# Kernel optimization log

Measured on AMD Instinct MI355X. Metric: run time of the kernel, lower is better.

The kernel has to match this reference:

```python
import jax, jax.numpy as jnp
import numpy as np

B, T, C, H = 4, 4096, 512, 64

def setup_inputs() -> dict:
    key = jax.random.key(0)
    kx, kk, kq, kv = jax.random.split(key, 4)
    return {
        "x": jax.random.normal(kx, (B, T, C), dtype=jnp.float32),
        "Wk": jax.random.normal(kk, (C, H), dtype=jnp.float32) * (C ** -0.5),
        "Wq": jax.random.normal(kq, (C, H), dtype=jnp.float32) * (C ** -0.5),
        "Wv": jax.random.normal(kv, (C, H), dtype=jnp.float32) * (C ** -0.5),
    }

def reference(x, Wk, Wq, Wv):
    # x: [B, T, C]; bias-free projections to head_size H
    k = x @ Wk  # [B, T, H]
    q = x @ Wq  # [B, T, H]
    v = x @ Wv  # [B, T, H]
    channels = x.shape[-1]
    # NOTE: original scales by channels**-0.5 (embedding dim), not head_size
    scale = jnp.asarray(channels, x.dtype) ** -0.5
    wei = jnp.einsum("bth,bsh->bts", q, k) * scale  # [B, T, T]
    t = x.shape[1]
    causal = jnp.tril(jnp.ones((t, t), dtype=bool))
    wei = jnp.where(causal, wei, -jnp.inf)
    wei = jax.nn.softmax(wei, axis=-1)
    out = jnp.einsum("bts,bsh->bth", wei, v)  # [B, T, H]
    return out
```

## Files before the change

kernel.cpp:

```cpp
#include <hip/hip_runtime.h>


typedef __attribute__((ext_vector_type(8))) __bf16 bf16x8;
typedef __attribute__((ext_vector_type(8))) unsigned short u16x8;
typedef __attribute__((ext_vector_type(4))) float f32x4;

#define B_ 4
#define T_ 4096
#define C_ 512
#define H_ 64
#define BT (B_ * T_)

#define QSCALE (0.04419417382415922f * 1.4426950408889634f)

__device__ __forceinline__ unsigned short f2bf(float f) {
    unsigned int u = __builtin_bit_cast(unsigned int, f);
    u += 0x7fffu + ((u >> 16) & 1u);
    return (unsigned short)(u >> 16);
}

__device__ __forceinline__ unsigned int pkbf(float hi, float lo) {
    return __builtin_amdgcn_perm(__builtin_bit_cast(unsigned int, hi),
                                 __builtin_bit_cast(unsigned int, lo), 0x07060302u);
}

__device__ __forceinline__ float bf2f_lo(unsigned int u) {
    return __builtin_bit_cast(float, u << 16);
}
__device__ __forceinline__ float bf2f_hi(unsigned int u) {
    return __builtin_bit_cast(float, u & 0xffff0000u);
}

__device__ __forceinline__ f32x4 mfma16(bf16x8 a, bf16x8 b, f32x4 c) {
    return __builtin_amdgcn_mfma_f32_16x16x32_bf16(a, b, c, 0, 0, 0);
}

__device__ __forceinline__ void gload_lds16(const void* g, void* lds_uniform) {
    __builtin_amdgcn_global_load_lds(
        (const __attribute__((address_space(1))) unsigned int*)g,
        (__attribute__((address_space(3))) unsigned int*)lds_uniform, 16, 0, 0);
}

__global__ __launch_bounds__(256) void wt_kernel(const float* __restrict__ Wk,
                                                 const float* __restrict__ Wq,
                                                 const float* __restrict__ Wv,
                                                 unsigned short* __restrict__ Wtp) {
    int gid = blockIdx.x * 256 + threadIdx.x;
    int fidx = gid >> 9;
    int li = gid & 511;
    int lane = li >> 3, j = li & 7;
    int m3 = fidx / 64;
    int rem = fidx & 63;
    int nt = rem >> 4, kc = rem & 15;
    int h = nt * 16 + (lane & 15);
    int c = kc * 32 + (lane >> 4) * 8 + j;
    const float* W = (m3 == 0) ? Wk : ((m3 == 1) ? Wq : Wv);
    Wtp[gid] = f2bf(W[c * H_ + h]);
}

__global__ __launch_bounds__(256, 3) void proj_kernel(const float* __restrict__ x,
                                                      const unsigned short* __restrict__ Wtp,
                                                      unsigned short* __restrict__ Kf,
                                                      unsigned short* __restrict__ Qf,
                                                      unsigned short* __restrict__ Vf) {
    __shared__ __align__(16) char smem[2 * 64 * 52 * 4];
    float* Mg = (float*)smem;
    unsigned short* Ks_l = (unsigned short*)smem;
    unsigned short* Qs_l = Ks_l + 32 * 68;
    unsigned short* Vt_l = Qs_l + 32 * 68;

    const int tid = threadIdx.x;
    const int t0 = blockIdx.x * 32;
    const int wave = tid >> 6;
    const int ws = wave & 1;
    const int wh = wave >> 1;
    const int lane = tid & 63;
    const int lane15 = lane & 15;
    const int quad = lane >> 4;

    f32x4 acc[12];
#pragma unroll
    for (int i = 0; i < 12; ++i) acc[i] = (f32x4){0.f, 0.f, 0.f, 0.f};

    const float* xrow = x + (long)(t0 + ws * 16 + lane15) * C_;
    const unsigned short* wbase = Wtp + lane * 8;

    bf16x8 wf[12];
    float4 xa0[2], xa1[2];
    {
        const int kc0 = wh * 8;
        xa0[0] = *(const float4*)(xrow + kc0 * 32 + quad * 8);
        xa1[0] = *(const float4*)(xrow + kc0 * 32 + quad * 8 + 4);
        xa0[1] = *(const float4*)(xrow + (kc0 + 1) * 32 + quad * 8);
        xa1[1] = *(const float4*)(xrow + (kc0 + 1) * 32 + quad * 8 + 4);
#pragma unroll
        for (int i = 0; i < 12; ++i)
            wf[i] = *(const bf16x8*)(wbase + ((i * 16 + kc0) << 9));
    }

#pragma unroll
    for (int kk = 0; kk < 8; ++kk) {
        const int kc = wh * 8 + kk;
        const int cur = kk & 1;
        u16x8 t;
        t[0] = f2bf(xa0[cur].x); t[1] = f2bf(xa0[cur].y);
        t[2] = f2bf(xa0[cur].z); t[3] = f2bf(xa0[cur].w);
        t[4] = f2bf(xa1[cur].x); t[5] = f2bf(xa1[cur].y);
        t[6] = f2bf(xa1[cur].z); t[7] = f2bf(xa1[cur].w);
        bf16x8 a = __builtin_bit_cast(bf16x8, t);
        if (kk < 6) {
            xa0[cur] = *(const float4*)(xrow + (kc + 2) * 32 + quad * 8);
            xa1[cur] = *(const float4*)(xrow + (kc + 2) * 32 + quad * 8 + 4);
        }
        __builtin_amdgcn_s_setprio(1);
#pragma unroll
        for (int i = 0; i < 12; ++i) {
            acc[i] = mfma16(a, wf[i], acc[i]);
            if (kk < 7)
                wf[i] = *(const bf16x8*)(wbase + ((i * 16 + kc + 1) << 9));
        }
        __builtin_amdgcn_s_setprio(0);
    }

    if (wh == 1) {
        float* mg = Mg + (ws * 64 + lane) * 52;
#pragma unroll
        for (int i = 0; i < 12; ++i) *(f32x4*)(mg + i * 4) = acc[i];
    }
    __syncthreads();
    if (wh == 0) {
        const float* mg = Mg + (ws * 64 + lane) * 52;
#pragma unroll
        for (int i = 0; i < 12; ++i) acc[i] += *(const f32x4*)(mg + i * 4);
    }
    __syncthreads();

    if (wh == 0) {
#pragma unroll
        for (int nt = 0; nt < 4; ++nt) {
            int col = nt * 16 + lane15;
#pragma unroll
            for (int r = 0; r < 4; ++r) {
                int row_l = ws * 16 + quad * 4 + r;
                Ks_l[row_l * 68 + col] = f2bf(acc[0 * 4 + nt][r]);
                Qs_l[row_l * 68 + col] = f2bf(acc[1 * 4 + nt][r] * QSCALE);
                Vt_l[col * 34 + row_l] = f2bf(acc[2 * 4 + nt][r]);
            }
        }
    }
    __syncthreads();

    const int b = t0 >> 12;
    const int tloc = t0 & 4095;
    const int st = wave >> 1, kk = wave & 1;
    const long gs = (long)(b * 256 + (tloc >> 4) + st);
    bf16x8 kv = *(const bf16x8*)&Ks_l[(st * 16 + lane15) * 68 + kk * 32 + quad * 8];
    *(bf16x8*)&Kf[(gs * 2 + kk) * 512 + lane * 8] = kv;
    bf16x8 qv = *(const bf16x8*)&Qs_l[(st * 16 + lane15) * 68 + kk * 32 + quad * 8];
    *(bf16x8*)&Qf[(gs * 2 + kk) * 512 + lane * 8] = qv;
    const int hf = wave;
    const int vkk = (tloc >> 5) & 1;
    bf16x8 vv = *(const bf16x8*)&Vt_l[(hf * 16 + lane15) * 34 + quad * 8];
    const long sb = (long)(b * 64 + (tloc >> 6));
    *(bf16x8*)&Vf[(sb * 8 + hf * 2 + vkk) * 512 + lane * 8] = vv;
}

#define PSP 72

__global__ __launch_bounds__(256, 3) void attn_kernel(const unsigned short* __restrict__ Qf,
                                                      const unsigned short* __restrict__ Kf,
                                                      const unsigned short* __restrict__ Vf,
                                                      unsigned short* __restrict__ Opb,
                                                      float* __restrict__ lp,
                                                      float* __restrict__ out) {
    __shared__ __align__(16) unsigned short KV[2][8192];
    __shared__ __align__(16) unsigned short Ps[8][16 * PSP];

    const int tid = threadIdx.x;
    const int wave = tid >> 6;
    const int lane = tid & 63;
    const int lane15 = lane & 15;
    const int quad = lane >> 4;
    const int b = blockIdx.y;

    const int z = 143 - blockIdx.x;
    int g = (int)((__builtin_sqrtf(2.0f * (float)z + 1.0f) - 1.0f) * 0.5f);
    while (2 * (g + 1) * (g + 2) <= z) ++g;
    while (2 * g * (g + 1) > z) --g;
    const int idx = z - 2 * g * (g + 1);
    const int qmt = g * 4 + idx / (g + 1);
    const int chunk = idx % (g + 1);
    const int ntt = min(8, 2 * qmt + 2 - chunk * 8);
    const int t0k = chunk * 8;
    const int dt0 = 2 * qmt, dt1 = 2 * qmt + 1;
    const int qg0 = qmt * 128 + wave * 16 + lane15;

    const long gq = (long)(b * 256 + qmt * 8 + wave);
    const unsigned short* qb = Qf + gq * 1024 + lane * 8;
    const bf16x8 qf00 = *(const bf16x8*)qb;
    const bf16x8 qf01 = *(const bf16x8*)(qb + 512);
    const bf16x8 qf10 = *(const bf16x8*)(qb + 4096);
    const bf16x8 qf11 = *(const bf16x8*)(qb + 4096 + 512);

    f32x4 o0[4], o1[4];
    f32x4 lv0 = (f32x4){0.f, 0.f, 0.f, 0.f};
    f32x4 lv1 = (f32x4){0.f, 0.f, 0.f, 0.f};
#pragma unroll
    for (int hf = 0; hf < 4; ++hf) {
        o0[hf] = (f32x4){0.f, 0.f, 0.f, 0.f};
        o1[hf] = (f32x4){0.f, 0.f, 0.f, 0.f};
    }

    const char* kbase = (const char*)Kf + ((long)(b * 256) << 11);
    const char* vbase = (const char*)Vf + ((long)(b * 64) << 13);
#define STAGE(kc_, buf_)                                                             \
    do {                                                                             \
        const char* ks_ = kbase + ((long)(kc_) << 13) + wave * 2048 + lane * 16;     \
        const char* vs_ = vbase + ((long)(kc_) << 13) + wave * 2048 + lane * 16;     \
        unsigned short* dk_ = &KV[buf_][wave * 1024];                                \
        unsigned short* dv_ = &KV[buf_][4096 + wave * 1024];                         \
        gload_lds16(ks_, dk_);                                                       \
        gload_lds16(ks_ + 1024, dk_ + 512);                                          \
        gload_lds16(vs_, dv_);                                                       \
        gload_lds16(vs_ + 1024, dv_ + 512);                                          \
    } while (0)

    STAGE(t0k, 0);
    if (ntt > 1) STAGE(t0k + 1, 1);

    unsigned short* pw0 = &Ps[wave * 2 + 0][0];
    unsigned short* pw1 = &Ps[wave * 2 + 1][0];

    for (int t = 0; t < ntt; ++t) {
        const int kc = t0k + t;
        const int buf = t & 1;
        if (t + 1 < ntt)
            asm volatile("s_waitcnt vmcnt(4)" ::: "memory");
        else
            asm volatile("s_waitcnt vmcnt(0)" ::: "memory");
        __builtin_amdgcn_sched_barrier(0);
        __builtin_amdgcn_s_barrier();

        const unsigned short* Kb = &KV[buf][0];
        const unsigned short* Vb = &KV[buf][4096];
        const int sbt = kc * 64;
        const bool do0 = (kc <= dt0);

        bf16x8 kf[8];
#pragma unroll
        for (int ct = 0; ct < 4; ++ct) {
            kf[ct * 2 + 0] = *(const bf16x8*)&Kb[ct * 1024 + lane * 8];
            kf[ct * 2 + 1] = *(const bf16x8*)&Kb[ct * 1024 + 512 + lane * 8];
        }

        if (do0) {
            f32x4 st[4];
            __builtin_amdgcn_s_setprio(1);
#pragma unroll
            for (int ct = 0; ct < 4; ++ct) {
                f32x4 zz = (f32x4){0.f, 0.f, 0.f, 0.f};
                zz = mfma16(kf[ct * 2 + 0], qf00, zz);
                zz = mfma16(kf[ct * 2 + 1], qf01, zz);
                st[ct] = zz;
            }
            __builtin_amdgcn_s_setprio(0);
            if (kc == dt0) {
#pragma unroll
                for (int ct = 0; ct < 4; ++ct) {
                    const int sb = sbt + ct * 16 + quad * 4;
#pragma unroll
                    for (int r = 0; r < 4; ++r)
                        if (sb + r > qg0) st[ct][r] = -3.0e38f;
                }
            }
#pragma unroll
            for (int ct = 0; ct < 4; ++ct) {
#pragma unroll
                for (int r = 0; r < 4; ++r)
                    st[ct][r] = __builtin_amdgcn_exp2f(st[ct][r]);
                lv0 += st[ct];
            }
#pragma unroll
            for (int ct = 0; ct < 4; ++ct) {
                unsigned int w0 = pkbf(st[ct][1], st[ct][0]);
                unsigned int w1 = pkbf(st[ct][3], st[ct][2]);
                *(uint2*)&pw0[lane15 * PSP + ct * 16 + quad * 4] = make_uint2(w0, w1);
            }
        }

        {
            f32x4 su[4];
            __builtin_amdgcn_s_setprio(1);
#pragma unroll
            for (int ct = 0; ct < 4; ++ct) {
                f32x4 zz = (f32x4){0.f, 0.f, 0.f, 0.f};
                zz = mfma16(kf[ct * 2 + 0], qf10, zz);
                zz = mfma16(kf[ct * 2 + 1], qf11, zz);
                su[ct] = zz;
            }
            __builtin_amdgcn_s_setprio(0);
            if (kc == dt1) {
                const int qg1 = qg0 + 64;
#pragma unroll
                for (int ct = 0; ct < 4; ++ct) {
                    const int sb = sbt + ct * 16 + quad * 4;
#pragma unroll
                    for (int r = 0; r < 4; ++r)
                        if (sb + r > qg1) su[ct][r] = -3.0e38f;
                }
            }
#pragma unroll
            for (int ct = 0; ct < 4; ++ct) {
#pragma unroll
                for (int r = 0; r < 4; ++r)
                    su[ct][r] = __builtin_amdgcn_exp2f(su[ct][r]);
                lv1 += su[ct];
            }
#pragma unroll
            for (int ct = 0; ct < 4; ++ct) {
                unsigned int w0 = pkbf(su[ct][1], su[ct][0]);
                unsigned int w1 = pkbf(su[ct][3], su[ct][2]);
                *(uint2*)&pw1[lane15 * PSP + ct * 16 + quad * 4] = make_uint2(w0, w1);
            }
        }

        bf16x8 vf[8];
#pragma unroll
        for (int f = 0; f < 8; ++f) vf[f] = *(const bf16x8*)&Vb[f * 512 + lane * 8];

        bf16x8 pa10 = *(const bf16x8*)&pw1[lane15 * PSP + quad * 8];
        bf16x8 pa11 = *(const bf16x8*)&pw1[lane15 * PSP + 32 + quad * 8];
        if (do0) {
            bf16x8 pa00 = *(const bf16x8*)&pw0[lane15 * PSP + quad * 8];
            bf16x8 pa01 = *(const bf16x8*)&pw0[lane15 * PSP + 32 + quad * 8];
            __builtin_amdgcn_s_setprio(1);
#pragma unroll
            for (int hf = 0; hf < 4; ++hf) {
                o0[hf] = mfma16(pa00, vf[hf * 2 + 0], o0[hf]);
                o0[hf] = mfma16(pa01, vf[hf * 2 + 1], o0[hf]);
            }
            __builtin_amdgcn_s_setprio(0);
        }
        __builtin_amdgcn_s_setprio(1);
#pragma unroll
        for (int hf = 0; hf < 4; ++hf) {
            o1[hf] = mfma16(pa10, vf[hf * 2 + 0], o1[hf]);
            o1[hf] = mfma16(pa11, vf[hf * 2 + 1], o1[hf]);
        }
        __builtin_amdgcn_s_setprio(0);

        __builtin_amdgcn_s_barrier();
        if (t + 2 < ntt) STAGE(t0k + t + 2, buf);
    }
#undef STAGE

    float l0 = (lv0[0] + lv0[1]) + (lv0[2] + lv0[3]);
    l0 += __shfl_xor(l0, 16);
    l0 += __shfl_xor(l0, 32);
    float l1 = (lv1[0] + lv1[1]) + (lv1[2] + lv1[3]);
    l1 += __shfl_xor(l1, 16);
    l1 += __shfl_xor(l1, 32);

    if (qmt < 4) {
        float linv0[4], linv1[4];
#pragma unroll
        for (int r = 0; r < 4; ++r) {
            linv0[r] = 1.0f / __shfl(l0, quad * 4 + r);
            linv1[r] = 1.0f / __shfl(l1, quad * 4 + r);
        }
        float* o = out + ((long)b * T_ + qmt * 128 + wave * 16) * H_;
#pragma unroll
        for (int hf = 0; hf < 4; ++hf)
#pragma unroll
            for (int r = 0; r < 4; ++r)
                o[(quad * 4 + r) * H_ + hf * 16 + lane15] = o0[hf][r] * linv0[r];
        float* o2 = o + 64 * H_;
#pragma unroll
        for (int hf = 0; hf < 4; ++hf)
#pragma unroll
            for (int r = 0; r < 4; ++r)
                o2[(quad * 4 + r) * H_ + hf * 16 + lane15] = o1[hf][r] * linv1[r];
    } else {
        const long pb0 = ((long)(b * 64 + dt0) * 8 + chunk) * 64;
        if (quad == 0) lp[pb0 + wave * 16 + lane15] = l0;
        unsigned short* op0 = Opb + (pb0 + wave * 16) * 64;
#pragma unroll
        for (int hf = 0; hf < 4; ++hf)
#pragma unroll
            for (int r = 0; r < 4; ++r)
                op0[(quad * 4 + r) * 64 + hf * 16 + lane15] = f2bf(o0[hf][r]);
        const long pb1 = ((long)(b * 64 + dt1) * 8 + chunk) * 64;
        if (quad == 0) lp[pb1 + wave * 16 + lane15] = l1;
        unsigned short* op1 = Opb + (pb1 + wave * 16) * 64;
#pragma unroll
        for (int hf = 0; hf < 4; ++hf)
#pragma unroll
            for (int r = 0; r < 4; ++r)
                op1[(quad * 4 + r) * 64 + hf * 16 + lane15] = f2bf(o1[hf][r]);
    }
}

__global__ __launch_bounds__(256) void merge_kernel(const unsigned short* __restrict__ Opb,
                                                    const float* __restrict__ lp,
                                                    float* __restrict__ out) {
    const int qt = 8 + (blockIdx.x >> 1);
    const int rh = (blockIdx.x & 1) << 5;
    const int b = blockIdx.y;
    const int nc = 1 + (qt >> 3);
    const int tid = threadIdx.x;
    const int row = rh + (tid >> 3);
    const int seg = (tid & 7) << 3;

    const long base = (long)(b * 64 + qt) * 8;
    float l = 0.f;
    f32x4 a0 = (f32x4){0.f, 0.f, 0.f, 0.f};
    f32x4 a1 = (f32x4){0.f, 0.f, 0.f, 0.f};

#pragma unroll 2
    for (int c = 0; c < nc; ++c) {
        l += lp[(base + c) * 64 + row];
        const unsigned short* op = Opb + ((base + c) * 64 + row) * 64 + seg;
        uint4 d = *(const uint4*)op;
        a0[0] += bf2f_lo(d.x); a0[1] += bf2f_hi(d.x);
        a0[2] += bf2f_lo(d.y); a0[3] += bf2f_hi(d.y);
        a1[0] += bf2f_lo(d.z); a1[1] += bf2f_hi(d.z);
        a1[2] += bf2f_lo(d.w); a1[3] += bf2f_hi(d.w);
    }
    const float inv = 1.0f / l;
    float* o = out + ((long)b * T_ + qt * 64 + row) * H_ + seg;
    *(f32x4*)o = a0 * inv;
    *(f32x4*)(o + 4) = a1 * inv;
}

extern "C" void kernel_launch(void* const* d_in, const int* in_sizes, int n_in,
                              void* d_out, int out_size, void* d_ws, size_t ws_size,
                              hipStream_t stream) {
    const float* x  = (const float*)d_in[0];
    const float* Wk = (const float*)d_in[1];
    const float* Wq = (const float*)d_in[2];
    const float* Wv = (const float*)d_in[3];
    float* out = (float*)d_out;

    char* ws = (char*)d_ws;
    unsigned short* Kf  = (unsigned short*)(ws);
    unsigned short* Qf  = (unsigned short*)(ws + (2u << 20));
    unsigned short* Vf  = (unsigned short*)(ws + (4u << 20));
    unsigned short* Wtp = (unsigned short*)(ws + (6u << 20));
    unsigned short* Opb = (unsigned short*)(ws + (8u << 20));
    float* lp = (float*)(ws + (26u << 20));

    wt_kernel<<<384, 256, 0, stream>>>(Wk, Wq, Wv, Wtp);
    proj_kernel<<<BT / 32, 256, 0, stream>>>(x, Wtp, Kf, Qf, Vf);
    attn_kernel<<<dim3(144, B_), 256, 0, stream>>>(Qf, Kf, Vf, Opb, lp, out);
    merge_kernel<<<dim3(112, B_), 256, 0, stream>>>(Opb, lp, out);
}
```

Baseline: 109.3 us.

## Fuse split-K merge into attention kernel via last-block atomic counter

Removes the separate merge kernel launch. Each attention block now bumps a per-query-tile atomic counter after writing its partial outputs, and the last block to finish for that tile reduces all chunk partials and writes the final output. The counters are zeroed in the weight-transpose kernel. This saves a kernel launch and its tail, but adds threadfences and atomics, and puts a serial reduction tail on the last-arriving blocks.

```diff
diff --git a/kernel.cpp b/kernel.cpp
--- a/kernel.cpp
+++ b/kernel.cpp
@@ -44,8 +44,10 @@
 __global__ __launch_bounds__(256) void wt_kernel(const float* __restrict__ Wk,
                                                  const float* __restrict__ Wq,
                                                  const float* __restrict__ Wv,
-                                                 unsigned short* __restrict__ Wtp) {
+                                                 unsigned short* __restrict__ Wtp,
+                                                 int* __restrict__ cnt) {
     int gid = blockIdx.x * 256 + threadIdx.x;
+    if (gid < 128) cnt[gid] = 0;
     int fidx = gid >> 9;
     int li = gid & 511;
     int lane = li >> 3, j = li & 7;
@@ -172,9 +174,11 @@
                                                       const unsigned short* __restrict__ Vf,
                                                       unsigned short* __restrict__ Opb,
                                                       float* __restrict__ lp,
+                                                      int* __restrict__ cnt,
                                                       float* __restrict__ out) {
     __shared__ __align__(16) unsigned short KV[2][8192];
     __shared__ __align__(16) unsigned short Ps[8][16 * PSP];
+    __shared__ int is_last;
 
     const int tid = threadIdx.x;
     const int wave = tid >> 6;
@@ -397,39 +401,43 @@
 #pragma unroll
             for (int r = 0; r < 4; ++r)
                 op1[(quad * 4 + r) * 64 + hf * 16 + lane15] = f2bf(o1[hf][r]);
-    }
-}
-
-__global__ __launch_bounds__(256) void merge_kernel(const unsigned short* __restrict__ Opb,
-                                                    const float* __restrict__ lp,
-                                                    float* __restrict__ out) {
-    const int qt = 8 + (blockIdx.x >> 1);
-    const int rh = (blockIdx.x & 1) << 5;
-    const int b = blockIdx.y;
-    const int nc = 1 + (qt >> 3);
-    const int tid = threadIdx.x;
-    const int row = rh + (tid >> 3);
-    const int seg = (tid & 7) << 3;
-
-    const long base = (long)(b * 64 + qt) * 8;
-    float l = 0.f;
-    f32x4 a0 = (f32x4){0.f, 0.f, 0.f, 0.f};
-    f32x4 a1 = (f32x4){0.f, 0.f, 0.f, 0.f};
-
-#pragma unroll 2
-    for (int c = 0; c < nc; ++c) {
-        l += lp[(base + c) * 64 + row];
-        const unsigned short* op = Opb + ((base + c) * 64 + row) * 64 + seg;
-        uint4 d = *(const uint4*)op;
-        a0[0] += bf2f_lo(d.x); a0[1] += bf2f_hi(d.x);
-        a0[2] += bf2f_lo(d.y); a0[3] += bf2f_hi(d.y);
-        a1[0] += bf2f_lo(d.z); a1[1] += bf2f_hi(d.z);
-        a1[2] += bf2f_lo(d.w); a1[3] += bf2f_hi(d.w);
-    }
-    const float inv = 1.0f / l;
-    float* o = out + ((long)b * T_ + qt * 64 + row) * H_ + seg;
-    *(f32x4*)o = a0 * inv;
-    *(f32x4*)(o + 4) = a1 * inv;
+
+        __threadfence();
+        __syncthreads();
+        if (tid == 0) {
+            int old = atomicAdd(&cnt[b * 32 + qmt], 1);
+            is_last = (old == g) ? 1 : 0;
+        }
+        __syncthreads();
+        if (is_last) {
+            __threadfence();
+            const int row128 = tid >> 1;
+            const int dt = dt0 + (row128 >> 6);
+            const int row = row128 & 63;
+            const int seg = (tid & 1) << 5;
+            const long mbase = (long)(b * 64 + dt) * 8;
+            float l = 0.f;
+            f32x4 a[8];
+#pragma unroll
+            for (int j = 0; j < 8; ++j) a[j] = (f32x4){0.f, 0.f, 0.f, 0.f};
+            for (int c = 0; c <= g; ++c) {
+                l += lp[(mbase + c) * 64 + row];
+                const unsigned short* op = Opb + ((mbase + c) * 64 + row) * 64 + seg;
+#pragma unroll
+                for (int j = 0; j < 4; ++j) {
+                    uint4 d = *(const uint4*)(op + j * 8);
+                    a[j * 2 + 0][0] += bf2f_lo(d.x); a[j * 2 + 0][1] += bf2f_hi(d.x);
+                    a[j * 2 + 0][2] += bf2f_lo(d.y); a[j * 2 + 0][3] += bf2f_hi(d.y);
+                    a[j * 2 + 1][0] += bf2f_lo(d.z); a[j * 2 + 1][1] += bf2f_hi(d.z);
+                    a[j * 2 + 1][2] += bf2f_lo(d.w); a[j * 2 + 1][3] += bf2f_hi(d.w);
+                }
+            }
+            const float inv = 1.0f / l;
+            float* o = out + ((long)b * T_ + dt * 64 + row) * H_ + seg;
+#pragma unroll
+            for (int j = 0; j < 8; ++j) *(f32x4*)(o + j * 4) = a[j] * inv;
+        }
+    }
 }
 
 extern "C" void kernel_launch(void* const* d_in, const int* in_sizes, int n_in,
@@ -448,9 +456,9 @@
     unsigned short* Wtp = (unsigned short*)(ws + (6u << 20));
     unsigned short* Opb = (unsigned short*)(ws + (8u << 20));
     float* lp = (float*)(ws + (26u << 20));
-
-    wt_kernel<<<384, 256, 0, stream>>>(Wk, Wq, Wv, Wtp);
+    int* cnt = (int*)(ws + (27u << 20));
+
+    wt_kernel<<<384, 256, 0, stream>>>(Wk, Wq, Wv, Wtp, cnt);
     proj_kernel<<<BT / 32, 256, 0, stream>>>(x, Wtp, Kf, Qf, Vf);
-    attn_kernel<<<dim3(144, B_), 256, 0, stream>>>(Qf, Kf, Vf, Opb, lp, out);
-    merge_kernel<<<dim3(112, B_), 256, 0, stream>>>(Opb, lp, out);
-}
+    attn_kernel<<<dim3(144, B_), 256, 0, stream>>>(Qf, Kf, Vf, Opb, lp, cnt, out);
+}
```

Result: slower. 215.5 us (+97.2%).
